# Optimization experiments

Hardware: AMD Instinct MI355X
Metric: run time of the kernel (lower is better)

Reference implementation:

```python
import jax, jax.numpy as jnp
import numpy as np

N_E = 8192
E_DIM = 256
BETA = 0.25


def setup_inputs() -> dict:
    key = jax.random.key(0)
    k1, k2 = jax.random.split(key)
    z = jax.random.normal(k1, (8, 64, 64, E_DIM), dtype=jnp.float32)
    # embedding init: uniform(-1/n_e, 1/n_e) as in the torch module
    emb = jax.random.uniform(k2, (N_E, E_DIM), dtype=jnp.float32,
                             minval=-1.0 / N_E, maxval=1.0 / N_E)
    return {"z": z, "emb": emb}


def reference(z, emb):
    sg = jax.lax.stop_gradient
    zf = z.reshape(-1, E_DIM)  # [N, D]
    # squared euclidean distance (argmin-equivalent to torch.cdist)
    # d[n,k] = ||zf[n]||^2 - 2 zf[n].e[k] + ||e[k]||^2
    d = (jnp.sum(zf * zf, axis=1, keepdims=True)
         - 2.0 * (zf @ emb.T)
         + jnp.sum(emb * emb, axis=1))  # [N, n_e]
    idx = jnp.argmin(d, axis=1)  # [N]
    z_q = emb[idx].reshape(z.shape)
    loss_commit = BETA * jnp.mean((sg(z_q) - z) ** 2)
    loss_codebook = jnp.mean((z_q - sg(z)) ** 2)
    z_q_ste = z + sg(z_q - z)  # straight-through estimator
    return z_q_ste, loss_commit, loss_codebook, idx
```

## Files before the change

### kernel.cpp

```cpp
#include <hip/hip_runtime.h>


#define NROWS 32768
#define NE    8192
#define DDIM  256
#define BM    64
#define CAP   64
#define MARGIN 1e-4f
#define NCH   (NE / 64)

typedef __attribute__((ext_vector_type(8))) short bf16x8;
typedef __attribute__((ext_vector_type(4))) float f32x4;
typedef unsigned short u16;

__device__ __forceinline__ u16 f2bf(float f) {
  unsigned x = __float_as_uint(f);
  return (u16)((x + 0x7fffu + ((x >> 16) & 1u)) >> 16);
}

__device__ __forceinline__ void gload_lds16(const void* g, void* l) {
  __builtin_amdgcn_global_load_lds(
      (const __attribute__((address_space(1))) void*)g,
      (__attribute__((address_space(3))) void*)l, 16, 0, 0);
}

__global__ __launch_bounds__(256)
void vq_norms(const float* __restrict__ z, const float* __restrict__ emb,
              float* __restrict__ arow, float* __restrict__ cemb) {
  int gid  = blockIdx.x * 256 + threadIdx.x;
  int wid  = gid >> 6;
  int lane = threadIdx.x & 63;
  const float* src;
  float* dst;
  if (wid < NROWS) { src = z + (size_t)wid * DDIM;   dst = arow + wid; }
  else             { int r = wid - NROWS;
                     src = emb + (size_t)r * DDIM;   dst = cemb + r; }
  float4 v = *reinterpret_cast<const float4*>(src + lane * 4);
  float s = v.x * v.x + v.y * v.y;
  s += v.z * v.z;
  s += v.w * v.w;
  #pragma unroll
  for (int off = 1; off < 64; off <<= 1) s += __shfl_xor(s, off, 64);
  if (lane == 0) *dst = s;
}

__global__ __launch_bounds__(256)
void vq_cvt(const float* __restrict__ emb, u16* __restrict__ e16) {
  int o   = blockIdx.x * 256 + threadIdx.x;
  int g16 = o >> 9;
  int r   = o & 511;
  int s   = r >> 6;
  int l   = r & 63;
  int lg  = l >> 4, l15 = l & 15;
  int c   = g16 * 16 + l15;
  int kc  = s * 4 + lg;
  const float* src = emb + (size_t)c * DDIM + kc * 8;
  float4 v0 = *reinterpret_cast<const float4*>(src);
  float4 v1 = *reinterpret_cast<const float4*>(src + 4);
  u16 ov[8] = {f2bf(v0.x), f2bf(v0.y), f2bf(v0.z), f2bf(v0.w),
               f2bf(v1.x), f2bf(v1.y), f2bf(v1.z), f2bf(v1.w)};
  *reinterpret_cast<bf16x8*>(e16 + (size_t)o * 8) =
      *reinterpret_cast<bf16x8*>(ov);
}

__global__ __launch_bounds__(512, 4)
void vq_mfma(const float* __restrict__ z, const u16* __restrict__ e16,
             const float* __restrict__ arow, const float* __restrict__ cemb,
             unsigned* __restrict__ cnt, int* __restrict__ list) {
  __shared__ u16 Bs[2][64 * DDIM];

  const int t    = threadIdx.x;
  const int R0   = blockIdx.x * BM;
  const int lane = t & 63;
  const int wid  = t >> 6;
  const int wm   = wid >> 1;
  const int wn   = wid & 1;
  const int l15  = lane & 15;
  const int lg   = lane >> 4;

  bf16x8 af[8];
  const int row = R0 + wm * 16 + l15;
  {
    const float* zr = z + (size_t)row * DDIM;
    #pragma unroll
    for (int s = 0; s < 8; ++s) {
      const float* src = zr + (s * 4 + lg) * 8;
      float4 v0 = *reinterpret_cast<const float4*>(src);
      float4 v1 = *reinterpret_cast<const float4*>(src + 4);
      u16 o[8] = {f2bf(v0.x), f2bf(v0.y), f2bf(v0.z), f2bf(v0.w),
                  f2bf(v1.x), f2bf(v1.y), f2bf(v1.z), f2bf(v1.w)};
      af[s] = *reinterpret_cast<bf16x8*>(o);
    }
  }
  const float a_r = arow[row];
  float runmin = 3.4e38f;

  {
    const char* src = (const char*)e16;
    #pragma unroll
    for (int i = 0; i < 4; ++i) {
      int f = wid * 4 + i;
      gload_lds16(src + f * 1024 + lane * 16, (char*)&Bs[0][0] + f * 1024);
    }
  }
  __syncthreads();

  for (int ch = 0; ch < NCH; ++ch) {
    const int buf = ch & 1;
    const int C0  = ch * 64;

    if (ch + 1 < NCH) {
      const char* src = (const char*)e16 + (size_t)(ch + 1) * 32768;
      char* dst = (char*)&Bs[buf ^ 1][0];
      #pragma unroll
      for (int i = 0; i < 4; ++i) {
        int f = wid * 4 + i;
        gload_lds16(src + f * 1024 + lane * 16, dst + f * 1024);
      }
    }

    float4 cvv[2];
    #pragma unroll
    for (int ci = 0; ci < 2; ++ci)
      cvv[ci] = *reinterpret_cast<const float4*>(
          &cemb[C0 + wn * 32 + ci * 16 + lg * 4]);

    f32x4 acc[2];
    acc[0] = (f32x4){0.f, 0.f, 0.f, 0.f};
    acc[1] = (f32x4){0.f, 0.f, 0.f, 0.f};

    const u16* Bp = &Bs[buf][0];
    #pragma unroll
    for (int s = 0; s < 8; ++s) {
      bf16x8 bfr[2];
      #pragma unroll
      for (int ci = 0; ci < 2; ++ci)
        bfr[ci] = *reinterpret_cast<const bf16x8*>(
            &Bp[((wn * 2 + ci) * 8 + s) * 512 + lane * 8]);
      #pragma unroll
      for (int ci = 0; ci < 2; ++ci)
        acc[ci] = __builtin_amdgcn_mfma_f32_16x16x32_bf16(
            bfr[ci], af[s], acc[ci], 0, 0, 0);
    }

    __syncthreads();

    float lm = 3.4e38f;
    #pragma unroll
    for (int ci = 0; ci < 2; ++ci)
      #pragma unroll
      for (int r = 0; r < 4; ++r) {
        float dd = fmaf(-2.0f, acc[ci][r], a_r) + cvv[ci][r];
        lm = fminf(lm, dd);
      }
    float gm = fminf(lm, __shfl_xor(lm, 16, 64));
    gm = fminf(gm, __shfl_xor(gm, 32, 64));
    runmin = fminf(runmin, gm);
    float thr = runmin + MARGIN;
    if (lm <= thr) {
      const float h = 0.5f * (a_r - thr);
      #pragma unroll
      for (int ci = 0; ci < 2; ++ci)
        #pragma unroll
        for (int r = 0; r < 4; ++r)
          if (acc[ci][r] >= fmaf(0.5f, cvv[ci][r], h)) {
            int k = C0 + wn * 32 + ci * 16 + lg * 4 + r;
            unsigned p = atomicAdd(&cnt[row], 1u);
            if (p < CAP) list[(size_t)row * CAP + p] = k;
          }
    }
  }
}

__global__ __launch_bounds__(256)
void vq_rescore(const float* __restrict__ z, const float* __restrict__ emb,
                const float* __restrict__ arow, const float* __restrict__ cemb,
                const unsigned* __restrict__ cnt, const int* __restrict__ list,
                int* __restrict__ ws_idx) {
  const int row  = blockIdx.x * 4 + (threadIdx.x >> 6);
  const int lane = threadIdx.x & 63;
  const float a  = arow[row];
  const float4 zv = *reinterpret_cast<const float4*>(
      z + (size_t)row * DDIM + lane * 4);
  unsigned n = cnt[row];
  float bd = 3.4e38f;
  int   bk = 0;

  const bool fullscan = (n == 0 || n > CAP);
  const int  m = fullscan ? NE : (int)n;
  for (int i = 0; i < m; ++i) {
    int k = fullscan ? i : list[(size_t)row * CAP + i];
    const float4 ev = *reinterpret_cast<const float4*>(
        emb + (size_t)k * DDIM + lane * 4);
    float p = zv.x * ev.x;
    p = fmaf(zv.y, ev.y, p);
    p = fmaf(zv.z, ev.z, p);
    p = fmaf(zv.w, ev.w, p);
    #pragma unroll
    for (int off = 1; off < 64; off <<= 1) p += __shfl_xor(p, off, 64);
    float d = fmaf(-2.0f, p, a) + cemb[k];
    if (d < bd || (d == bd && k < bk)) { bd = d; bk = k; }
  }
  if (lane == 0) ws_idx[row] = bk;
}

__global__ __launch_bounds__(256)
void vq_gather(const float* __restrict__ z, const float* __restrict__ emb,
               const int* __restrict__ ws_idx,
               float* __restrict__ out_zq, float* __restrict__ out_idx,
               double* __restrict__ loss_accum) {
  __shared__ float part[4];
  const int t  = threadIdx.x;
  const int R0 = blockIdx.x * 64;
  float lsum = 0.0f;
  for (int rr = 0; rr < 64; ++rr) {
    const int kb = ws_idx[R0 + rr];
    const size_t gi = (size_t)(R0 + rr) * DDIM + t;
    const float zv = z[gi];
    const float qv = emb[(size_t)kb * DDIM + t];
    const float diff = qv - zv;
    out_zq[gi] = zv + diff;
    lsum = fmaf(diff, diff, lsum);
  }
  #pragma unroll
  for (int off = 1; off < 64; off <<= 1) lsum += __shfl_xor(lsum, off, 64);
  if ((t & 63) == 0) part[t >> 6] = lsum;
  __syncthreads();
  if (t == 0) {
    float tot = (part[0] + part[1]) + (part[2] + part[3]);
    atomicAdd(loss_accum, (double)tot);
  }
  if (t < 64) out_idx[R0 + t] = (float)ws_idx[R0 + t];
}

__global__ void vq_finalize(const double* __restrict__ loss_accum,
                            float* __restrict__ out_losses) {
  double m = *loss_accum / (double)((size_t)NROWS * DDIM);
  out_losses[0] = (float)(0.25 * m);
  out_losses[1] = (float)m;
}

extern "C" void kernel_launch(void* const* d_in, const int* in_sizes, int n_in,
                              void* d_out, int out_size, void* d_ws, size_t ws_size,
                              hipStream_t stream) {
  const float* z   = (const float*)d_in[0];
  const float* emb = (const float*)d_in[1];
  float* out        = (float*)d_out;
  float* out_zq     = out;
  float* out_losses = out + (size_t)NROWS * DDIM;
  float* out_idx    = out + (size_t)NROWS * DDIM + 2;

  double* loss_accum = (double*)d_ws;
  float*  arow   = (float*)((char*)d_ws + 256);
  float*  cemb   = arow + NROWS;
  int*    ws_idx = (int*)(cemb + NE);

  u16*      e16  = (u16*)d_out;
  int*      list = (int*)((char*)d_out + (4 << 20));
  unsigned* cnt  = (unsigned*)((char*)d_out + (12 << 20));

  hipMemsetAsync(d_ws, 0, 8, stream);
  hipMemsetAsync(cnt, 0, NROWS * sizeof(unsigned), stream);
  vq_norms<<<(NROWS + NE) / 4, 256, 0, stream>>>(z, emb, arow, cemb);
  vq_cvt<<<NE * 32 / 256, 256, 0, stream>>>(emb, e16);
  vq_mfma<<<NROWS / BM, 512, 0, stream>>>(z, e16, arow, cemb, cnt, list);
  vq_rescore<<<NROWS / 4, 256, 0, stream>>>(z, emb, arow, cemb, cnt, list, ws_idx);
  vq_gather<<<NROWS / 64, 256, 0, stream>>>(z, emb, ws_idx,
                                            out_zq, out_idx, loss_accum);
  vq_finalize<<<1, 1, 0, stream>>>(loss_accum, out_losses);
}
```

Measured before the change: 321.5 us.

## Fuse rescore with gather and loss, spread loss atomics over 256 slots

When the workspace is large enough, scratch buffers move from the output into the workspace, so the rescore kernel can write z_q, the index and the loss partials directly. This drops the separate gather kernel, the ws_idx round trip and the single-slot double atomic, which is replaced by 256 partial slots reduced in a small finalize kernel. The fallback gather path is also vectorized to float4 per wavefront row. Whether the fused path runs depends on the harness providing at least 14 MB of workspace.

```diff
diff --git a/kernel.cpp b/kernel.cpp
--- a/kernel.cpp
+++ b/kernel.cpp
@@ -173,6 +173,90 @@
 }
 
 __global__ __launch_bounds__(256)
+void vq_rescore_fused(const float* __restrict__ z, const float* __restrict__ emb,
+                      const float* __restrict__ arow, const float* __restrict__ cemb,
+                      const unsigned* __restrict__ cnt, const int* __restrict__ list,
+                      float* __restrict__ out_zq, float* __restrict__ out_idx,
+                      double* __restrict__ part) {
+  __shared__ float part4[4];
+  const int wid  = threadIdx.x >> 6;
+  const int row  = blockIdx.x * 4 + wid;
+  const int lane = threadIdx.x & 63;
+  const float a  = arow[row];
+  const float4 zv = *reinterpret_cast<const float4*>(
+      z + (size_t)row * DDIM + lane * 4);
+  unsigned n = cnt[row];
+  float bd = 3.4e38f;
+  int   bk = 0;
+
+  if (n != 0 && n <= CAP) {
+    for (int i = 0; i < (int)n; ++i) {
+      int k = list[(size_t)row * CAP + i];
+      const float4 ev = *reinterpret_cast<const float4*>(
+          emb + (size_t)k * DDIM + lane * 4);
+      float p = zv.x * ev.x;
+      p = fmaf(zv.y, ev.y, p);
+      p = fmaf(zv.z, ev.z, p);
+      p = fmaf(zv.w, ev.w, p);
+      #pragma unroll
+      for (int off = 1; off < 64; off <<= 1) p += __shfl_xor(p, off, 64);
+      float d = fmaf(-2.0f, p, a) + cemb[k];
+      if (d < bd || (d == bd && k < bk)) { bd = d; bk = k; }
+    }
+  } else {
+    for (int i = 0; i < NE; ++i) {
+      const float4 ev = *reinterpret_cast<const float4*>(
+          emb + (size_t)i * DDIM + lane * 4);
+      float p = zv.x * ev.x;
+      p = fmaf(zv.y, ev.y, p);
+      p = fmaf(zv.z, ev.z, p);
+      p = fmaf(zv.w, ev.w, p);
+      #pragma unroll
+      for (int off = 1; off < 64; off <<= 1) p += __shfl_xor(p, off, 64);
+      float d = fmaf(-2.0f, p, a) + cemb[i];
+      if (d < bd) { bd = d; bk = i; }
+    }
+  }
+
+  const float4 ev = *reinterpret_cast<const float4*>(
+      emb + (size_t)bk * DDIM + lane * 4);
+  float dx = ev.x - zv.x;
+  float dy = ev.y - zv.y;
+  float dz = ev.z - zv.z;
+  float dw = ev.w - zv.w;
+  float4 o = {zv.x + dx, zv.y + dy, zv.z + dz, zv.w + dw};
+  *reinterpret_cast<float4*>(out_zq + (size_t)row * DDIM + lane * 4) = o;
+  float lsum = dx * dx;
+  lsum = fmaf(dy, dy, lsum);
+  lsum = fmaf(dz, dz, lsum);
+  lsum = fmaf(dw, dw, lsum);
+  #pragma unroll
+  for (int off = 1; off < 64; off <<= 1) lsum += __shfl_xor(lsum, off, 64);
+  if (lane == 0) {
+    part4[wid] = lsum;
+    out_idx[row] = (float)bk;
+  }
+  __syncthreads();
+  if (threadIdx.x == 0) {
+    float tot = (part4[0] + part4[1]) + (part4[2] + part4[3]);
+    atomicAdd(&part[blockIdx.x & 255], (double)tot);
+  }
+}
+
+__global__ void vq_finalize_fused(const double* __restrict__ part,
+                                  float* __restrict__ out_losses) {
+  int lane = threadIdx.x & 63;
+  double s = part[lane] + part[lane + 64] + part[lane + 128] + part[lane + 192];
+  #pragma unroll
+  for (int off = 1; off < 64; off <<= 1) s += __shfl_xor(s, off, 64);
+  if (lane == 0) {
+    double m = s / (double)((size_t)NROWS * DDIM);
+    out_losses[0] = (float)(0.25 * m);
+    out_losses[1] = (float)m;
+  }
+}
+
+__global__ __launch_bounds__(256)
 void vq_rescore(const float* __restrict__ z, const float* __restrict__ emb,
                 const float* __restrict__ arow, const float* __restrict__ cemb,
                 const unsigned* __restrict__ cnt, const int* __restrict__ list,
@@ -185,7 +269,6 @@
   unsigned n = cnt[row];
   float bd = 3.4e38f;
   int   bk = 0;
-
   const bool fullscan = (n == 0 || n > CAP);
   const int  m = fullscan ? NE : (int)n;
   for (int i = 0; i < m; ++i) {
@@ -210,21 +293,32 @@
                float* __restrict__ out_zq, float* __restrict__ out_idx,
                double* __restrict__ loss_accum) {
   __shared__ float part[4];
-  const int t  = threadIdx.x;
-  const int R0 = blockIdx.x * 64;
+  const int t    = threadIdx.x;
+  const int wid  = t >> 6;
+  const int lane = t & 63;
+  const int R0   = blockIdx.x * 64;
   float lsum = 0.0f;
-  for (int rr = 0; rr < 64; ++rr) {
-    const int kb = ws_idx[R0 + rr];
-    const size_t gi = (size_t)(R0 + rr) * DDIM + t;
-    const float zv = z[gi];
-    const float qv = emb[(size_t)kb * DDIM + t];
-    const float diff = qv - zv;
-    out_zq[gi] = zv + diff;
-    lsum = fmaf(diff, diff, lsum);
+  for (int rr = 0; rr < 16; ++rr) {
+    const int row = R0 + rr * 4 + wid;
+    const int kb  = ws_idx[row];
+    const float4 zv = *reinterpret_cast<const float4*>(
+        z + (size_t)row * DDIM + lane * 4);
+    const float4 ev = *reinterpret_cast<const float4*>(
+        emb + (size_t)kb * DDIM + lane * 4);
+    float dx = ev.x - zv.x;
+    float dy = ev.y - zv.y;
+    float dz = ev.z - zv.z;
+    float dw = ev.w - zv.w;
+    float4 o = {zv.x + dx, zv.y + dy, zv.z + dz, zv.w + dw};
+    *reinterpret_cast<float4*>(out_zq + (size_t)row * DDIM + lane * 4) = o;
+    lsum = fmaf(dx, dx, lsum);
+    lsum = fmaf(dy, dy, lsum);
+    lsum = fmaf(dz, dz, lsum);
+    lsum = fmaf(dw, dw, lsum);
   }
   #pragma unroll
   for (int off = 1; off < 64; off <<= 1) lsum += __shfl_xor(lsum, off, 64);
-  if ((t & 63) == 0) part[t >> 6] = lsum;
+  if (lane == 0) part[wid] = lsum;
   __syncthreads();
   if (t == 0) {
     float tot = (part[0] + part[1]) + (part[2] + part[3]);
@@ -250,22 +344,45 @@
   float* out_losses = out + (size_t)NROWS * DDIM;
   float* out_idx    = out + (size_t)NROWS * DDIM + 2;
 
-  double* loss_accum = (double*)d_ws;
-  float*  arow   = (float*)((char*)d_ws + 256);
-  float*  cemb   = arow + NROWS;
-  int*    ws_idx = (int*)(cemb + NE);
-
-  u16*      e16  = (u16*)d_out;
-  int*      list = (int*)((char*)d_out + (4 << 20));
-  unsigned* cnt  = (unsigned*)((char*)d_out + (12 << 20));
-
-  hipMemsetAsync(d_ws, 0, 8, stream);
-  hipMemsetAsync(cnt, 0, NROWS * sizeof(unsigned), stream);
-  vq_norms<<<(NROWS + NE) / 4, 256, 0, stream>>>(z, emb, arow, cemb);
-  vq_cvt<<<NE * 32 / 256, 256, 0, stream>>>(emb, e16);
-  vq_mfma<<<NROWS / BM, 512, 0, stream>>>(z, e16, arow, cemb, cnt, list);
-  vq_rescore<<<NROWS / 4, 256, 0, stream>>>(z, emb, arow, cemb, cnt, list, ws_idx);
-  vq_gather<<<NROWS / 64, 256, 0, stream>>>(z, emb, ws_idx,
-                                            out_zq, out_idx, loss_accum);
-  vq_finalize<<<1, 1, 0, stream>>>(loss_accum, out_losses);
-}
+  const bool big_ws = ws_size >= (size_t)(14u << 20);
+
+  if (big_ws) {
+    char* w = (char*)d_ws;
+    double*   part = (double*)w;
+    float*    arow = (float*)(w + 4096);
+    float*    cemb = (float*)(w + 4096 + 131072);
+    unsigned* cnt  = (unsigned*)(w + 4096 + 131072 + 32768);
+    u16*      e16  = (u16*)(w + (1u << 20));
+    int*      list = (int*)(w + (5u << 20));
+
+    hipMemsetAsync(part, 0, 2048, stream);
+    hipMemsetAsync(cnt, 0, NROWS * sizeof(unsigned), stream);
+    vq_norms<<<(NROWS + NE) / 4, 256, 0, stream>>>(z, emb, arow, cemb);
+    vq_cvt<<<NE * 32 / 256, 256, 0, stream>>>(emb, e16);
+    vq_mfma<<<NROWS / BM, 512, 0, stream>>>(z, e16, arow, cemb, cnt, list);
+    vq_rescore_fused<<<NROWS / 4, 256, 0, stream>>>(z, emb, arow, cemb,
+                                                    cnt, list,
+                                                    out_zq, out_idx, part);
+    vq_finalize_fused<<<1, 64, 0, stream>>>(part, out_losses);
+  } else {
+    double* loss_accum = (double*)d_ws;
+    float*  arow   = (float*)((char*)d_ws + 256);
+    float*  cemb   = arow + NROWS;
+    int*    ws_idx = (int*)(cemb + NE);
+
+    u16*      e16  = (u16*)d_out;
+    int*      list = (int*)((char*)d_out + (4 << 20));
+    unsigned* cnt  = (unsigned*)((char*)d_out + (12 << 20));
+
+    hipMemsetAsync(d_ws, 0, 8, stream);
+    hipMemsetAsync(cnt, 0, NROWS * sizeof(unsigned), stream);
+    vq_norms<<<(NROWS + NE) / 4, 256, 0, stream>>>(z, emb, arow, cemb);
+    vq_cvt<<<NE * 32 / 256, 256, 0, stream>>>(emb, e16);
+    vq_mfma<<<NROWS / BM, 512, 0, stream>>>(z, e16, arow, cemb, cnt, list);
+    vq_rescore<<<NROWS / 4, 256, 0, stream>>>(z, emb, arow, cemb, cnt, list,
+                                              ws_idx);
+    vq_gather<<<NROWS / 64, 256, 0, stream>>>(z, emb, ws_idx,
+                                              out_zq, out_idx, loss_accum);
+    vq_finalize<<<1, 1, 0, stream>>>(loss_accum, out_losses);
+  }
+}
```

After: 308.4 us. -4.1%, faster.
